# Optimization experiments

Measured on AMD Instinct MI355X. Metric: run time of the kernel, lower is better.

Reference implementation:

```python
import jax, jax.numpy as jnp
import numpy as np

B, D = 8192, 128
TEMP = 0.07
EPS = 1e-12  # F.normalize default eps (clamp on norm)


def _l2norm(x):
    n = jnp.sqrt(jnp.sum(x * x, axis=1, keepdims=True))
    return x / jnp.maximum(n, EPS)


def setup_inputs() -> dict:
    key = jax.random.key(0)
    k1, k2, k3, k4 = jax.random.split(key, 4)
    return {
        "feat_fv": jax.random.normal(k1, (B, D), dtype=jnp.float32),
        "feat_fi": jax.random.normal(k2, (B, D), dtype=jnp.float32),
        "feat_v": jax.random.normal(k3, (B, D), dtype=jnp.float32),
        "feat_i": jax.random.normal(k4, (B, D), dtype=jnp.float32),
    }


def reference(feat_fv, feat_fi, feat_v, feat_i):
    fv = _l2norm(feat_fv)
    fi = _l2norm(feat_fi)
    v = _l2norm(feat_v)
    vi = _l2norm(feat_i)

    # positive logits: per-sample dot products [B]
    pos_v = jnp.sum(fv * v, axis=1)
    pos_i = jnp.sum(fi * vi, axis=1)
    use_v = pos_v >= pos_i                      # branch condition per row
    pos = jnp.where(use_v, pos_v, pos_i)        # [B]

    # full pairwise dot products, branch-select per row
    Sv = jnp.einsum('bd,kd->bk', fv, v)         # [B, B]
    Si = jnp.einsum('bd,kd->bk', fi, vi)        # [B, B]
    S = jnp.where(use_v[:, None], Sv, Si)       # [B, B]

    n = S.shape[0]
    diag = jnp.eye(n, dtype=bool)
    # negatives exclude the positive (diagonal) entry -> mask to -inf
    neg_logits = jnp.where(diag, -jnp.inf, S / TEMP)  # [B, B]

    # cross-entropy with target class 0 (the positive), reduction='none':
    # loss_b = logsumexp([pos/T, negs/T]) - pos/T
    lse = jnp.logaddexp(pos / TEMP, jax.scipy.special.logsumexp(neg_logits, axis=1))
    return lse - pos / TEMP
```

## Files before the change

kernel.cpp:

```cpp
#include <hip/hip_runtime.h>
#include <math.h>

#define Bsz 8192
#define Dd  128
#define BM  64
#define NSLICE 8
#define ROT2(x) ((((x) << 2) | ((x) >> 4)) & 63)

typedef __attribute__((ext_vector_type(8))) short short8;
typedef __attribute__((ext_vector_type(4))) float float4v;

static constexpr float INV_T = 1.0f / 0.07f;

static __device__ inline unsigned pack_bf16(float x, float y) {
    union { float f; unsigned u; } a, b;
    a.f = x; b.f = y;
    unsigned ra = a.u + 0x7FFF + ((a.u >> 16) & 1);
    unsigned rb = b.u + 0x7FFF + ((b.u >> 16) & 1);
    return (ra >> 16) | (rb & 0xFFFF0000u);
}

__global__ void init_kernel(unsigned long long* __restrict__ cnt) {
    if (threadIdx.x == 0) cnt[0] = 0ull;
}

__global__ __launch_bounds__(1024) void prep_kernel(
    const float4* __restrict__ fv4, const float4* __restrict__ fi4,
    const float4* __restrict__ v4,  const float4* __restrict__ vi4,
    unsigned* __restrict__ Xb, uint2* __restrict__ Yf0, uint2* __restrict__ Yf1,
    float* __restrict__ posArr, int* __restrict__ origArr, int* __restrict__ flagArr,
    float* __restrict__ lAcc, unsigned long long* __restrict__ cnt)
{
    __shared__ unsigned sT0[32 * 66];
    __shared__ unsigned sT1[32 * 66];
    __shared__ int sFlagL[32];
    __shared__ int sRank[32];
    __shared__ unsigned sBase[2];

    const int t    = threadIdx.x;
    const int wave = t >> 6;
    const int lane = t & 63;
    const int half = lane >> 5;
    const int c    = lane & 31;
    const int rl   = wave * 2 + half;
    const int b    = blockIdx.x * 32 + rl;
    const int src  = b * 32 + c;

    const float4 afv = fv4[src];
    const float4 afi = fi4[src];
    const float4 av  = v4[src];
    const float4 avi = vi4[src];

    float nfv = afv.x*afv.x + afv.y*afv.y + afv.z*afv.z + afv.w*afv.w;
    float nfi = afi.x*afi.x + afi.y*afi.y + afi.z*afi.z + afi.w*afi.w;
    float nv  = av.x*av.x   + av.y*av.y   + av.z*av.z   + av.w*av.w;
    float nvi = avi.x*avi.x + avi.y*avi.y + avi.z*avi.z + avi.w*avi.w;
    float dv  = afv.x*av.x  + afv.y*av.y  + afv.z*av.z  + afv.w*av.w;
    float di  = afi.x*avi.x + afi.y*avi.y + afi.z*avi.z + afi.w*avi.w;

    #pragma unroll
    for (int m = 1; m < 32; m <<= 1) {
        nfv += __shfl_xor(nfv, m);
        nfi += __shfl_xor(nfi, m);
        nv  += __shfl_xor(nv,  m);
        nvi += __shfl_xor(nvi, m);
        dv  += __shfl_xor(dv,  m);
        di  += __shfl_xor(di,  m);
    }

    const float rnfv = 1.0f / fmaxf(sqrtf(nfv), 1e-12f);
    const float rnfi = 1.0f / fmaxf(sqrtf(nfi), 1e-12f);
    const float rnv  = 1.0f / fmaxf(sqrtf(nv ), 1e-12f);
    const float rnvi = 1.0f / fmaxf(sqrtf(nvi), 1e-12f);

    const float pos_v = dv * rnfv * rnv;
    const float pos_i = di * rnfi * rnvi;
    const bool useV = (pos_v >= pos_i);
    const float pos = useV ? pos_v : pos_i;

    uint2 w0y = make_uint2(pack_bf16(av.x  * rnv,  av.y  * rnv),
                           pack_bf16(av.z  * rnv,  av.w  * rnv));
    uint2 w1y = make_uint2(pack_bf16(avi.x * rnvi, avi.y * rnvi),
                           pack_bf16(avi.z * rnvi, avi.w * rnvi));
    *(uint2*)&sT0[rl * 66 + c * 2] = w0y;
    *(uint2*)&sT1[rl * 66 + c * 2] = w1y;
    if (c == 0) sFlagL[rl] = useV ? 0 : 1;
    __syncthreads();

    if (t < 64) {
        const int f = (lane < 32) ? sFlagL[lane] : 2;
        const unsigned long long m0 = __ballot(f == 0);
        const unsigned long long m1 = __ballot(f == 1);
        if (lane == 0) {
            const unsigned long long add =
                (unsigned long long)__popcll(m0) | ((unsigned long long)__popcll(m1) << 32);
            const unsigned long long ret = atomicAdd(cnt, add);
            sBase[0] = (unsigned)(ret & 0xffffffffull);
            sBase[1] = (unsigned)(ret >> 32);
        }
        if (lane < 32) {
            const unsigned long long below = (1ull << lane) - 1ull;
            sRank[lane] = (f == 0) ? (int)__popcll(m0 & below) : (int)__popcll(m1 & below);
        }
    }

    {
        const int tl = t >> 9;
        const int kc = (t >> 7) & 3;
        const int lp = (t >> 1) & 63;
        const int w0 = (t & 1) * 2;
        const int row = tl * 16 + (lp & 15);
        const int s   = kc * 16 + (lp >> 4) * 4 + w0;
        Yf0[blockIdx.x * 1024 + t] = *(const uint2*)&sT0[row * 66 + s];
        Yf1[blockIdx.x * 1024 + t] = *(const uint2*)&sT1[row * 66 + s];
    }
    __syncthreads();

    const int f  = sFlagL[rl];
    const int rk = sRank[rl];
    const int p  = (f == 0) ? (int)(sBase[0] + rk) : (Bsz - 1 - (int)(sBase[1] + rk));

    const float sc = useV ? rnfv : rnfi;
    ((uint2*)Xb)[p * 32 + c] = make_uint2(pack_bf16(afv.x * sc, afv.y * sc),
                                          pack_bf16(afv.z * sc, afv.w * sc));
    if (!useV)
        ((uint2*)Xb)[p * 32 + c] = make_uint2(pack_bf16(afi.x * sc, afi.y * sc),
                                              pack_bf16(afi.z * sc, afi.w * sc));

    if (c == 0) {
        posArr[p]  = pos;
        origArr[p] = b;
        flagArr[p] = f;
        lAcc[p]    = 0.0f;
    }
}

__global__ __launch_bounds__(256, 4) void main_kernel(
    const unsigned short* __restrict__ Xb,
    const uint4* __restrict__ Yf0q, const uint4* __restrict__ Yf1q,
    const int* __restrict__ flagArr, float* __restrict__ lAcc)
{
    __shared__ uint4 sXf[1024];
    __shared__ int sFlag[BM];
    __shared__ int sHas[2];

    const int t    = threadIdx.x;
    const int wave = t >> 6;
    const int lane = t & 63;
    const int quad = lane >> 4;
    const int mrow = lane & 15;
    const int slice = blockIdx.x & 7;
    const int p0    = (blockIdx.x >> 3) * BM;

    if (t < 2) sHas[t] = 0;
    __syncthreads();
    if (t < BM) {
        const int f = flagArr[p0 + t];
        sFlag[t] = f;
        atomicOr(&sHas[f], 1);
    }

    #pragma unroll
    for (int it = 0; it < 4; ++it) {
        const int i = t + it * 256;
        const int row = i >> 4, ch = i & 15;
        const uint4 val = ((const uint4*)Xb)[(p0 + row) * 16 + ch];
        const int blk16 = (row >> 4) * 4 + (ch >> 2);
        const int slot  = (ch & 3) * 16 + (row & 15);
        sXf[blk16 * 64 + ROT2(slot)] = val;
    }
    __syncthreads();

    short8 afr[4][4];
    #pragma unroll
    for (int rt = 0; rt < 4; ++rt)
        #pragma unroll
        for (int kc = 0; kc < 4; ++kc)
            afr[rt][kc] = *(const short8*)&sXf[(rt * 4 + kc) * 64 + ROT2(lane)];

    unsigned frmask = 0;
    #pragma unroll
    for (int rt = 0; rt < 4; ++rt)
        #pragma unroll
        for (int r = 0; r < 4; ++r)
            frmask |= (unsigned)sFlag[rt * 16 + quad * 4 + r] << (rt * 4 + r);

    float rowsum[4][4] = {};
    const int g0 = slice * 64 + wave * 16;

    for (int phase = 0; phase < 2; ++phase) {
        if (!sHas[phase]) continue;
        const uint4* __restrict__ yb = (phase ? Yf1q : Yf0q) + (size_t)g0 * 256 + lane;

        short8 b0 = *(const short8*)&yb[0];
        short8 b1 = *(const short8*)&yb[64];
        short8 b2 = *(const short8*)&yb[128];
        short8 b3 = *(const short8*)&yb[192];

        #pragma unroll 1
        for (int jt = 0; jt < 16; ++jt) {
            float4v acc[4] = {};
            #pragma unroll
            for (int rt = 0; rt < 4; ++rt)
                acc[rt] = __builtin_amdgcn_mfma_f32_16x16x32_bf16(afr[rt][0], b0, acc[rt], 0, 0, 0);
            #pragma unroll
            for (int rt = 0; rt < 4; ++rt)
                acc[rt] = __builtin_amdgcn_mfma_f32_16x16x32_bf16(afr[rt][1], b1, acc[rt], 0, 0, 0);
            if (jt < 15) {
                b0 = *(const short8*)&yb[256];
                b1 = *(const short8*)&yb[320];
            }
            #pragma unroll
            for (int rt = 0; rt < 4; ++rt)
                acc[rt] = __builtin_amdgcn_mfma_f32_16x16x32_bf16(afr[rt][2], b2, acc[rt], 0, 0, 0);
            #pragma unroll
            for (int rt = 0; rt < 4; ++rt)
                acc[rt] = __builtin_amdgcn_mfma_f32_16x16x32_bf16(afr[rt][3], b3, acc[rt], 0, 0, 0);
            if (jt < 15) {
                b2 = *(const short8*)&yb[384];
                b3 = *(const short8*)&yb[448];
            }
            yb += 256;

            #pragma unroll
            for (int rt = 0; rt < 4; ++rt)
                #pragma unroll
                for (int r = 0; r < 4; ++r)
                    if ((int)((frmask >> (rt * 4 + r)) & 1u) == phase)
                        rowsum[rt][r] += __expf(acc[rt][r] * INV_T - INV_T);
        }
    }

    #pragma unroll
    for (int m = 1; m < 16; m <<= 1)
        #pragma unroll
        for (int rt = 0; rt < 4; ++rt)
            #pragma unroll
            for (int r = 0; r < 4; ++r)
                rowsum[rt][r] += __shfl_xor(rowsum[rt][r], m);

    if (mrow == 0) {
        #pragma unroll
        for (int rt = 0; rt < 4; ++rt)
            #pragma unroll
            for (int r = 0; r < 4; ++r)
                atomicAdd(&lAcc[p0 + rt * 16 + quad * 4 + r], rowsum[rt][r]);
    }
}

__global__ __launch_bounds__(256) void finish_kernel(
    const float* __restrict__ lAcc, const float* __restrict__ posArr,
    const int* __restrict__ origArr, float* __restrict__ out)
{
    const int p = blockIdx.x * 256 + threadIdx.x;
    out[origArr[p]] = logf(lAcc[p]) + INV_T - posArr[p] * INV_T;
}

extern "C" void kernel_launch(void* const* d_in, const int* in_sizes, int n_in,
                              void* d_out, int out_size, void* d_ws, size_t ws_size,
                              hipStream_t stream)
{
    const float4* fv = (const float4*)d_in[0];
    const float4* fi = (const float4*)d_in[1];
    const float4* v  = (const float4*)d_in[2];
    const float4* vi = (const float4*)d_in[3];
    float* out = (float*)d_out;

    unsigned short* Xb  = (unsigned short*)d_ws;
    unsigned short* Yf0 = Xb  + Bsz * Dd;
    unsigned short* Yf1 = Yf0 + Bsz * Dd;
    float* posArr = (float*)(Yf1 + Bsz * Dd);
    float* lAcc   = posArr + Bsz;
    int*  origArr = (int*)(lAcc + Bsz);
    int*  flagArr = origArr + Bsz;
    unsigned long long* cnt = (unsigned long long*)(flagArr + Bsz);

    hipLaunchKernelGGL(init_kernel, dim3(1), dim3(64), 0, stream, cnt);
    hipLaunchKernelGGL(prep_kernel, dim3(Bsz / 32), dim3(1024), 0, stream,
                       fv, fi, v, vi, (unsigned*)Xb, (uint2*)Yf0, (uint2*)Yf1,
                       posArr, origArr, flagArr, lAcc, cnt);
    hipLaunchKernelGGL(main_kernel, dim3((Bsz / BM) * NSLICE), dim3(256), 0, stream,
                       Xb, (const uint4*)Yf0, (const uint4*)Yf1, flagArr, lAcc);
    hipLaunchKernelGGL(finish_kernel, dim3(Bsz / 256), dim3(256), 0, stream,
                       lAcc, posArr, origArr, out);
}
```

Before: 107.2 us.

## Fuse prep, main and finish into one cooperative kernel with XCD-aware slicing

Replaces the four kernel launches with a single cooperative kernel that uses grid-wide syncs between the prep, partition, GEMM/exp and finish stages. The atomic row-partition counter becomes a per-block count array with a deterministic prefix sum. In the main stage each 1024-thread block handles four 64-row tiles and picks its column slice from the hardware XCC id, so each XCD reuses the same Y slice in its L2. The goal is to cut launch gaps and improve cache locality, at the cost of grid-sync overhead, a fixed 256-block grid and a 1024-thread block size that may limit occupancy.

```diff
diff --git a/kernel.cpp b/kernel.cpp
--- a/kernel.cpp
+++ b/kernel.cpp
@@ -1,10 +1,10 @@
 #include <hip/hip_runtime.h>
+#include <hip/hip_cooperative_groups.h>
 #include <math.h>
 
+namespace cg = cooperative_groups;
+
 #define Bsz 8192
-#define Dd  128
-#define BM  64
-#define NSLICE 8
 #define ROT2(x) ((((x) << 2) | ((x) >> 4)) & 63)
 
 typedef __attribute__((ext_vector_type(8))) short short8;
@@ -20,31 +20,37 @@
     return (ra >> 16) | (rb & 0xFFFF0000u);
 }
 
-__global__ void init_kernel(unsigned long long* __restrict__ cnt) {
-    if (threadIdx.x == 0) cnt[0] = 0ull;
-}
-
-__global__ __launch_bounds__(1024) void prep_kernel(
+__global__ __launch_bounds__(1024, 4) void fused_kernel(
     const float4* __restrict__ fv4, const float4* __restrict__ fi4,
     const float4* __restrict__ v4,  const float4* __restrict__ vi4,
-    unsigned* __restrict__ Xb, uint2* __restrict__ Yf0, uint2* __restrict__ Yf1,
+    uint2* __restrict__ Xb2, uint2* __restrict__ Yf0, uint2* __restrict__ Yf1,
     float* __restrict__ posArr, int* __restrict__ origArr, int* __restrict__ flagArr,
-    float* __restrict__ lAcc, unsigned long long* __restrict__ cnt)
+    float* __restrict__ lAcc, float* __restrict__ out,
+    int* __restrict__ cntArr, int* __restrict__ xcdCnt)
 {
-    __shared__ unsigned sT0[32 * 66];
-    __shared__ unsigned sT1[32 * 66];
+    __shared__ union {
+        struct { unsigned T0[32 * 66]; unsigned T1[32 * 66]; } a;
+        struct { uint4 Xf[4][1024]; } c;
+        char pad[86016];
+    } U;
     __shared__ int sFlagL[32];
     __shared__ int sRank[32];
-    __shared__ unsigned sBase[2];
+    __shared__ int sPre;
+    __shared__ int sRkx;
+    __shared__ int sFlagC[4][64];
+    __shared__ int sHasC[4][2];
 
     const int t    = threadIdx.x;
+    const int pb   = blockIdx.x;
     const int wave = t >> 6;
     const int lane = t & 63;
     const int half = lane >> 5;
     const int c    = lane & 31;
     const int rl   = wave * 2 + half;
-    const int b    = blockIdx.x * 32 + rl;
+    const int b    = pb * 32 + rl;
     const int src  = b * 32 + c;
+
+    if (pb == 0 && t < 8) xcdCnt[t] = 0;
 
     const float4 afv = fv4[src];
     const float4 afi = fi4[src];
@@ -77,13 +83,12 @@
     const float pos_i = di * rnfi * rnvi;
     const bool useV = (pos_v >= pos_i);
     const float pos = useV ? pos_v : pos_i;
-
-    uint2 w0y = make_uint2(pack_bf16(av.x  * rnv,  av.y  * rnv),
-                           pack_bf16(av.z  * rnv,  av.w  * rnv));
-    uint2 w1y = make_uint2(pack_bf16(avi.x * rnvi, avi.y * rnvi),
-                           pack_bf16(avi.z * rnvi, avi.w * rnvi));
-    *(uint2*)&sT0[rl * 66 + c * 2] = w0y;
-    *(uint2*)&sT1[rl * 66 + c * 2] = w1y;
+    const float sc  = useV ? rnfv : rnfi;
+
+    *(uint2*)&U.a.T0[rl * 66 + c * 2] =
+        make_uint2(pack_bf16(av.x * rnv,  av.y * rnv),  pack_bf16(av.z * rnv,  av.w * rnv));
+    *(uint2*)&U.a.T1[rl * 66 + c * 2] =
+        make_uint2(pack_bf16(avi.x * rnvi, avi.y * rnvi), pack_bf16(avi.z * rnvi, avi.w * rnvi));
     if (c == 0) sFlagL[rl] = useV ? 0 : 1;
     __syncthreads();
 
@@ -91,19 +96,12 @@
         const int f = (lane < 32) ? sFlagL[lane] : 2;
         const unsigned long long m0 = __ballot(f == 0);
         const unsigned long long m1 = __ballot(f == 1);
-        if (lane == 0) {
-            const unsigned long long add =
-                (unsigned long long)__popcll(m0) | ((unsigned long long)__popcll(m1) << 32);
-            const unsigned long long ret = atomicAdd(cnt, add);
-            sBase[0] = (unsigned)(ret & 0xffffffffull);
-            sBase[1] = (unsigned)(ret >> 32);
-        }
+        if (lane == 0) cntArr[pb] = (int)__popcll(m0);
         if (lane < 32) {
             const unsigned long long below = (1ull << lane) - 1ull;
             sRank[lane] = (f == 0) ? (int)__popcll(m0 & below) : (int)__popcll(m1 & below);
         }
     }
-
     {
         const int tl = t >> 9;
         const int kc = (t >> 7) & 3;
@@ -111,63 +109,72 @@
         const int w0 = (t & 1) * 2;
         const int row = tl * 16 + (lp & 15);
         const int s   = kc * 16 + (lp >> 4) * 4 + w0;
-        Yf0[blockIdx.x * 1024 + t] = *(const uint2*)&sT0[row * 66 + s];
-        Yf1[blockIdx.x * 1024 + t] = *(const uint2*)&sT1[row * 66 + s];
-    }
-    __syncthreads();
-
-    const int f  = sFlagL[rl];
+        Yf0[pb * 1024 + t] = *(const uint2*)&U.a.T0[row * 66 + s];
+        Yf1[pb * 1024 + t] = *(const uint2*)&U.a.T1[row * 66 + s];
+    }
+
+    cg::this_grid().sync();
+
+    if (t < 64) {
+        int s = 0;
+        #pragma unroll
+        for (int j = 0; j < 4; ++j) {
+            const int idx2 = lane + j * 64;
+            if (idx2 < pb) s += cntArr[idx2];
+        }
+        #pragma unroll
+        for (int m = 1; m < 64; m <<= 1) s += __shfl_xor(s, m);
+        if (lane == 0) sPre = s;
+    }
+    __syncthreads();
+
+    const int f0 = useV ? 0 : 1;
     const int rk = sRank[rl];
-    const int p  = (f == 0) ? (int)(sBase[0] + rk) : (Bsz - 1 - (int)(sBase[1] + rk));
-
-    const float sc = useV ? rnfv : rnfi;
-    ((uint2*)Xb)[p * 32 + c] = make_uint2(pack_bf16(afv.x * sc, afv.y * sc),
-                                          pack_bf16(afv.z * sc, afv.w * sc));
-    if (!useV)
-        ((uint2*)Xb)[p * 32 + c] = make_uint2(pack_bf16(afi.x * sc, afi.y * sc),
-                                              pack_bf16(afi.z * sc, afi.w * sc));
-
+    const int pre0 = sPre;
+    const int p = (f0 == 0) ? (pre0 + rk)
+                            : (Bsz - 1 - (32 * pb - pre0 + rk));
+
+    const float4 ax = useV ? fv4[src] : fi4[src];
+    Xb2[p * 32 + c] = make_uint2(pack_bf16(ax.x * sc, ax.y * sc),
+                                 pack_bf16(ax.z * sc, ax.w * sc));
     if (c == 0) {
         posArr[p]  = pos;
         origArr[p] = b;
-        flagArr[p] = f;
+        flagArr[p] = f0;
         lAcc[p]    = 0.0f;
     }
-}
-
-__global__ __launch_bounds__(256, 4) void main_kernel(
-    const unsigned short* __restrict__ Xb,
-    const uint4* __restrict__ Yf0q, const uint4* __restrict__ Yf1q,
-    const int* __restrict__ flagArr, float* __restrict__ lAcc)
-{
-    __shared__ uint4 sXf[1024];
-    __shared__ int sFlag[BM];
-    __shared__ int sHas[2];
-
-    const int t    = threadIdx.x;
-    const int wave = t >> 6;
-    const int lane = t & 63;
+
+    cg::this_grid().sync();
+
+    unsigned xcc;
+    asm volatile("s_getreg_b32 %0, hwreg(HW_REG_XCC_ID)" : "=s"(xcc));
+    xcc &= 7;
+    if (t == 0) sRkx = atomicAdd(&xcdCnt[xcc], 1);
+    if (t < 8) sHasC[t >> 1][t & 1] = 0;
+    __syncthreads();
+
+    const int vb = t >> 8;
+    const int tl = t & 255;
+    const int wl = (t >> 6) & 3;
     const int quad = lane >> 4;
     const int mrow = lane & 15;
-    const int slice = blockIdx.x & 7;
-    const int p0    = (blockIdx.x >> 3) * BM;
-
-    if (t < 2) sHas[t] = 0;
-    __syncthreads();
-    if (t < BM) {
-        const int f = flagArr[p0 + t];
-        sFlag[t] = f;
-        atomicOr(&sHas[f], 1);
-    }
-
+    const int rowblk = sRkx * 4 + vb;
+    const int p0 = rowblk * 64;
+    const int slice = (int)xcc;
+
+    if (tl < 64) {
+        const int ff = flagArr[p0 + tl];
+        sFlagC[vb][tl] = ff;
+        atomicOr(&sHasC[vb][ff], 1);
+    }
     #pragma unroll
     for (int it = 0; it < 4; ++it) {
-        const int i = t + it * 256;
+        const int i = tl + it * 256;
         const int row = i >> 4, ch = i & 15;
-        const uint4 val = ((const uint4*)Xb)[(p0 + row) * 16 + ch];
+        const uint4 val = ((const uint4*)Xb2)[(p0 + row) * 16 + ch];
         const int blk16 = (row >> 4) * 4 + (ch >> 2);
         const int slot  = (ch & 3) * 16 + (row & 15);
-        sXf[blk16 * 64 + ROT2(slot)] = val;
+        U.c.Xf[vb][blk16 * 64 + ROT2(slot)] = val;
     }
     __syncthreads();
 
@@ -176,21 +183,22 @@
     for (int rt = 0; rt < 4; ++rt)
         #pragma unroll
         for (int kc = 0; kc < 4; ++kc)
-            afr[rt][kc] = *(const short8*)&sXf[(rt * 4 + kc) * 64 + ROT2(lane)];
+            afr[rt][kc] = *(const short8*)&U.c.Xf[vb][(rt * 4 + kc) * 64 + ROT2(lane)];
 
     unsigned frmask = 0;
     #pragma unroll
     for (int rt = 0; rt < 4; ++rt)
         #pragma unroll
         for (int r = 0; r < 4; ++r)
-            frmask |= (unsigned)sFlag[rt * 16 + quad * 4 + r] << (rt * 4 + r);
+            frmask |= (unsigned)sFlagC[vb][rt * 16 + quad * 4 + r] << (rt * 4 + r);
 
     float rowsum[4][4] = {};
-    const int g0 = slice * 64 + wave * 16;
+    const int g0 = slice * 64 + wl * 16;
 
     for (int phase = 0; phase < 2; ++phase) {
-        if (!sHas[phase]) continue;
-        const uint4* __restrict__ yb = (phase ? Yf1q : Yf0q) + (size_t)g0 * 256 + lane;
+        if (!sHasC[vb][phase]) continue;
+        const uint4* __restrict__ yb =
+            (const uint4*)(phase ? Yf1 : Yf0) + (size_t)g0 * 256 + lane;
 
         short8 b0 = *(const short8*)&yb[0];
         short8 b1 = *(const short8*)&yb[64];
@@ -206,28 +214,23 @@
             #pragma unroll
             for (int rt = 0; rt < 4; ++rt)
                 acc[rt] = __builtin_amdgcn_mfma_f32_16x16x32_bf16(afr[rt][1], b1, acc[rt], 0, 0, 0);
-            if (jt < 15) {
-                b0 = *(const short8*)&yb[256];
-                b1 = *(const short8*)&yb[320];
-            }
+            if (jt < 15) { b0 = *(const short8*)&yb[256]; b1 = *(const short8*)&yb[320]; }
             #pragma unroll
             for (int rt = 0; rt < 4; ++rt)
                 acc[rt] = __builtin_amdgcn_mfma_f32_16x16x32_bf16(afr[rt][2], b2, acc[rt], 0, 0, 0);
             #pragma unroll
             for (int rt = 0; rt < 4; ++rt)
                 acc[rt] = __builtin_amdgcn_mfma_f32_16x16x32_bf16(afr[rt][3], b3, acc[rt], 0, 0, 0);
-            if (jt < 15) {
-                b2 = *(const short8*)&yb[384];
-                b3 = *(const short8*)&yb[448];
-            }
+            if (jt < 15) { b2 = *(const short8*)&yb[384]; b3 = *(const short8*)&yb[448]; }
             yb += 256;
 
             #pragma unroll
             for (int rt = 0; rt < 4; ++rt)
                 #pragma unroll
-                for (int r = 0; r < 4; ++r)
-                    if ((int)((frmask >> (rt * 4 + r)) & 1u) == phase)
-                        rowsum[rt][r] += __expf(acc[rt][r] * INV_T - INV_T);
+                for (int r = 0; r < 4; ++r) {
+                    const float e = __expf(acc[rt][r] * INV_T - INV_T);
+                    rowsum[rt][r] += ((int)((frmask >> (rt * 4 + r)) & 1u) == phase) ? e : 0.0f;
+                }
         }
     }
 
@@ -246,14 +249,13 @@
             for (int r = 0; r < 4; ++r)
                 atomicAdd(&lAcc[p0 + rt * 16 + quad * 4 + r], rowsum[rt][r]);
     }
-}
-
-__global__ __launch_bounds__(256) void finish_kernel(
-    const float* __restrict__ lAcc, const float* __restrict__ posArr,
-    const int* __restrict__ origArr, float* __restrict__ out)
-{
-    const int p = blockIdx.x * 256 + threadIdx.x;
-    out[origArr[p]] = logf(lAcc[p]) + INV_T - posArr[p] * INV_T;
+
+    cg::this_grid().sync();
+
+    if (t < 32) {
+        const int p2 = pb * 32 + t;
+        out[origArr[p2]] = logf(lAcc[p2]) + INV_T - posArr[p2] * INV_T;
+    }
 }
 
 extern "C" void kernel_launch(void* const* d_in, const int* in_sizes, int n_in,
@@ -266,21 +268,26 @@
     const float4* vi = (const float4*)d_in[3];
     float* out = (float*)d_out;
 
-    unsigned short* Xb  = (unsigned short*)d_ws;
-    unsigned short* Yf0 = Xb  + Bsz * Dd;
-    unsigned short* Yf1 = Yf0 + Bsz * Dd;
-    float* posArr = (float*)(Yf1 + Bsz * Dd);
+    unsigned short* XbU  = (unsigned short*)d_ws;
+    unsigned short* Yf0U = XbU  + Bsz * 128;
+    unsigned short* Yf1U = Yf0U + Bsz * 128;
+    float* posArr = (float*)(Yf1U + Bsz * 128);
     float* lAcc   = posArr + Bsz;
     int*  origArr = (int*)(lAcc + Bsz);
     int*  flagArr = origArr + Bsz;
-    unsigned long long* cnt = (unsigned long long*)(flagArr + Bsz);
-
-    hipLaunchKernelGGL(init_kernel, dim3(1), dim3(64), 0, stream, cnt);
-    hipLaunchKernelGGL(prep_kernel, dim3(Bsz / 32), dim3(1024), 0, stream,
-                       fv, fi, v, vi, (unsigned*)Xb, (uint2*)Yf0, (uint2*)Yf1,
-                       posArr, origArr, flagArr, lAcc, cnt);
-    hipLaunchKernelGGL(main_kernel, dim3((Bsz / BM) * NSLICE), dim3(256), 0, stream,
-                       Xb, (const uint4*)Yf0, (const uint4*)Yf1, flagArr, lAcc);
-    hipLaunchKernelGGL(finish_kernel, dim3(Bsz / 256), dim3(256), 0, stream,
-                       lAcc, posArr, origArr, out);
+    int*  cntArr  = flagArr + Bsz;
+    int*  xcdCnt  = cntArr + 256;
+
+    uint2* Xb2 = (uint2*)XbU;
+    uint2* Yf0 = (uint2*)Yf0U;
+    uint2* Yf1 = (uint2*)Yf1U;
+
+    void* kargs[] = {
+        (void*)&fv, (void*)&fi, (void*)&v, (void*)&vi,
+        (void*)&Xb2, (void*)&Yf0, (void*)&Yf1,
+        (void*)&posArr, (void*)&origArr, (void*)&flagArr,
+        (void*)&lAcc, (void*)&out, (void*)&cntArr, (void*)&xcdCnt
+    };
+    hipLaunchCooperativeKernel((void*)fused_kernel, dim3(256), dim3(1024),
+                               kargs, 0, stream);
 }
```

After: 216.2 us. 2.02x slower.
